# Kernel tuning notes

Hardware: AMD Instinct MI355X
Metric: run time of the kernel (lower is better)

The kernel has to match this reference:

```python
import jax, jax.numpy as jnp
import numpy as np

B = 8192
D_LS, D_A, D_LM, D_AT, D_DS, D_DM = 1024, 512, 512, 512, 1024, 512
LENGTH = D_LS + D_A + D_LM  # 2048
OUT = 512


def setup_inputs() -> dict:
    key = jax.random.key(0)
    ks = jax.random.split(key, 9)
    return {
        "result_ls": jax.random.normal(ks[0], (B, 1, D_LS), jnp.float32),
        "result_A": jax.random.normal(ks[1], (B, 1, D_A), jnp.float32),
        "result_lm": jax.random.normal(ks[2], (B, 1, D_LM), jnp.float32),
        "result_AT": jax.random.normal(ks[3], (B, 1, D_AT), jnp.float32),
        "result_ds": jax.random.normal(ks[4], (B, 1, D_DS), jnp.float32),
        "result_dm": jax.random.normal(ks[5], (B, 1, D_DM), jnp.float32),
        "W": jax.random.normal(ks[6], (OUT, LENGTH), jnp.float32) * (1.0 / np.sqrt(LENGTH)),
        "b": jax.random.normal(ks[7], (OUT,), jnp.float32) * 0.01,
        "h_n": jax.random.normal(ks[8], (OUT, 1), jnp.float32) * (1.0 / np.sqrt(OUT)),
    }


def _pad_to(x, length):
    # zero-pad last dim of [B,1,d] to [B,1,length]
    return jnp.pad(x, ((0, 0), (0, 0), (0, length - x.shape[2])))


def reference(result_ls, result_A, result_lm, result_AT, result_ds, result_dm, W, b, h_n):
    # pad each node-type feature to common length and stack along node axis -> [B,6,L]
    nodes = jnp.concatenate(
        [_pad_to(t, LENGTH) for t in (result_ls, result_A, result_lm, result_AT, result_ds, result_dm)],
        axis=1,
    )
    temp = jnp.tanh(jnp.einsum("bnl,ol->bno", nodes, W) + b)  # [B,6,OUT]
    score = jnp.einsum("bno,oi->bni", temp, h_n)               # [B,6,1]
    score = score.reshape(-1, 1, 6)
    beta = jax.nn.softmax(score, axis=2)                        # [B,1,6]
    z_i = jnp.matmul(beta, nodes)                               # [B,1,L]
    return z_i
```

## Files before the change

### kernel.cpp

```cpp
#include <hip/hip_runtime.h>
#include <hip/hip_bf16.h>
#include <stdint.h>

typedef __attribute__((ext_vector_type(8))) short bf16x8;
typedef __attribute__((ext_vector_type(4))) float f32x4;

#define NB 8192

__device__ __forceinline__ unsigned pkbf(float x, float y) {
    __hip_bfloat162 h = __float22bfloat162_rn(make_float2(x, y));
    unsigned r;
    __builtin_memcpy(&r, &h, 4);
    return r;
}

__device__ __forceinline__ uint4 pack8(float4 a, float4 b) {
    uint4 r;
    r.x = pkbf(a.x, a.y);
    r.y = pkbf(a.z, a.w);
    r.z = pkbf(b.x, b.y);
    r.w = pkbf(b.z, b.w);
    return r;
}

__global__ __launch_bounds__(256)
void prep_w_kernel(const float* __restrict__ W, uint4* __restrict__ Wt) {
    int t = blockIdx.x * 256 + threadIdx.x;
    int lane = t & 63;
    int frag = t >> 6;
    int kb = frag >> 5, cb = frag & 31;
    int o = cb * 16 + (lane & 15);
    int k = kb * 32 + ((lane >> 4) << 3);
    const float* src = W + (size_t)o * 2048 + k;
    Wt[t] = pack8(*(const float4*)src, *(const float4*)(src + 4));
}

template<int DN>
__device__ __forceinline__ void score_body(
        const float* __restrict__ xp, int node, int tile,
        const float* __restrict__ bias, const float* __restrict__ hvec,
        const uint4* __restrict__ Wt, float* __restrict__ scores,
        uint4* lA, float* red) {
    constexpr int NKH = DN / 512;
    int t = threadIdx.x;
    int l = t & 63;
    int w = t >> 6;
    int m0 = tile << 6;

    f32x4 acc[4][4];
#pragma unroll
    for (int mf = 0; mf < 4; ++mf)
#pragma unroll
        for (int nf = 0; nf < 4; ++nf)
            acc[mf][nf] = (f32x4){0.f, 0.f, 0.f, 0.f};

    for (int kh = 0; kh < NKH; ++kh) {
        if (kh > 0) __syncthreads();
#pragma unroll
        for (int j = 0; j < 8; ++j) {
            int f = (t >> 6) + (j << 3);
            int row = (f & 3) * 16 + (l & 15);
            int k = (kh << 9) + ((f >> 2) << 5) + ((l >> 4) << 3);
            const float* g = xp + (size_t)(m0 + row) * DN + k;
            lA[(f << 6) + l] = pack8(*(const float4*)g, *(const float4*)(g + 4));
        }
        __syncthreads();

        int kbh0 = w << 1;
        uint4 bB[2][4], aA[2][4];
        {
            int kbh = kbh0 & 15;
            const uint4* wp = Wt + ((((kh << 4) + kbh) * 32 + (w << 2)) << 6) + l;
#pragma unroll
            for (int nf = 0; nf < 4; ++nf) bB[0][nf] = wp[nf << 6];
#pragma unroll
            for (int mf = 0; mf < 4; ++mf) aA[0][mf] = lA[(((kbh << 2) + mf) << 6) + l];
        }
#pragma unroll
        for (int i = 0; i < 16; ++i) {
            int cur = i & 1, nxt = cur ^ 1;
            if (i < 15) {
                int kbh = (kbh0 + i + 1) & 15;
                const uint4* wp = Wt + ((((kh << 4) + kbh) * 32 + (w << 2)) << 6) + l;
#pragma unroll
                for (int nf = 0; nf < 4; ++nf) bB[nxt][nf] = wp[nf << 6];
#pragma unroll
                for (int mf = 0; mf < 4; ++mf) aA[nxt][mf] = lA[(((kbh << 2) + mf) << 6) + l];
            }
#pragma unroll
            for (int mf = 0; mf < 4; ++mf) {
                bf16x8 afr;
                __builtin_memcpy(&afr, &aA[cur][mf], 16);
#pragma unroll
                for (int nf = 0; nf < 4; ++nf) {
                    bf16x8 bfr;
                    __builtin_memcpy(&bfr, &bB[cur][nf], 16);
                    acc[mf][nf] = __builtin_amdgcn_mfma_f32_16x16x32_bf16(
                        afr, bfr, acc[mf][nf], 0, 0, 0);
                }
            }
        }
    }

    float bv[4], hv[4];
#pragma unroll
    for (int nf = 0; nf < 4; ++nf) {
        int o = (w << 6) + (nf << 4) + (l & 15);
        bv[nf] = bias[o];
        hv[nf] = hvec[o];
    }
#pragma unroll
    for (int mf = 0; mf < 4; ++mf) {
        float sc[4] = {0.f, 0.f, 0.f, 0.f};
#pragma unroll
        for (int nf = 0; nf < 4; ++nf) {
#pragma unroll
            for (int r = 0; r < 4; ++r) {
                float xv = acc[mf][nf][r] + bv[nf];
                float th = 1.f - 2.f * __builtin_amdgcn_rcpf(1.f + __expf(2.f * xv));
                sc[r] = fmaf(hv[nf], th, sc[r]);
            }
        }
#pragma unroll
        for (int r = 0; r < 4; ++r) {
            float v = sc[r];
            v += __shfl_xor(v, 1);
            v += __shfl_xor(v, 2);
            v += __shfl_xor(v, 4);
            v += __shfl_xor(v, 8);
            if ((l & 15) == 0)
                red[(w << 6) + (mf << 4) + ((l >> 4) << 2) + r] = v;
        }
    }
    __syncthreads();
    if (t < 64) {
        float ssum = 0.f;
#pragma unroll
        for (int w2 = 0; w2 < 8; ++w2) ssum += red[(w2 << 6) + t];
        scores[node * NB + m0 + t] = ssum;
    }
}

__global__ __launch_bounds__(512)
void score_kernel(const float* __restrict__ x0, const float* __restrict__ x1,
                  const float* __restrict__ x2, const float* __restrict__ x3,
                  const float* __restrict__ x4, const float* __restrict__ x5,
                  const float* __restrict__ bias, const float* __restrict__ hvec,
                  const uint4* __restrict__ Wt, float* __restrict__ scores) {
    __shared__ uint4 lA[4096];
    __shared__ float red[8 * 64];
    int bid = blockIdx.x;
    int node = bid % 6;
    int tile = bid / 6;
    switch (node) {
        case 0: score_body<1024>(x0, 0, tile, bias, hvec, Wt, scores, lA, red); break;
        case 1: score_body<512>(x1, 1, tile, bias, hvec, Wt, scores, lA, red); break;
        case 2: score_body<512>(x2, 2, tile, bias, hvec, Wt, scores, lA, red); break;
        case 3: score_body<512>(x3, 3, tile, bias, hvec, Wt, scores, lA, red); break;
        case 4: score_body<1024>(x4, 4, tile, bias, hvec, Wt, scores, lA, red); break;
        default: score_body<512>(x5, 5, tile, bias, hvec, Wt, scores, lA, red); break;
    }
}

__global__ __launch_bounds__(256)
void z_kernel(const float* __restrict__ x0, const float* __restrict__ x1,
              const float* __restrict__ x2, const float* __restrict__ x3,
              const float* __restrict__ x4, const float* __restrict__ x5,
              const float* __restrict__ scores, float* __restrict__ out) {
    int wv = threadIdx.x >> 6;
    int lane = threadIdx.x & 63;
    int b = (blockIdx.x << 2) + wv;

    float s0 = scores[b];
    float s1 = scores[NB + b];
    float s2 = scores[2 * NB + b];
    float s3 = scores[3 * NB + b];
    float s4 = scores[4 * NB + b];
    float s5 = scores[5 * NB + b];
    float m = fmaxf(fmaxf(fmaxf(s0, s1), fmaxf(s2, s3)), fmaxf(s4, s5));
    float e0 = __expf(s0 - m), e1 = __expf(s1 - m), e2 = __expf(s2 - m);
    float e3 = __expf(s3 - m), e4 = __expf(s4 - m), e5 = __expf(s5 - m);
    float inv = __builtin_amdgcn_rcpf(e0 + e1 + e2 + e3 + e4 + e5);
    float b0 = e0 * inv, b1 = e1 * inv, b2 = e2 * inv;
    float b3 = e3 * inv, b4 = e4 * inv, b5 = e5 * inv;

    const float* pls = x0 + (size_t)b * 1024;
    const float* pA  = x1 + (size_t)b * 512;
    const float* plm = x2 + (size_t)b * 512;
    const float* pAT = x3 + (size_t)b * 512;
    const float* pds = x4 + (size_t)b * 1024;
    const float* pdm = x5 + (size_t)b * 512;
    float* po = out + (size_t)b * 2048;

#pragma unroll
    for (int j = 0; j < 2; ++j) {
        int c = (j << 8) + (lane << 2);
        float4 vls = *(const float4*)(pls + c);
        float4 vA  = *(const float4*)(pA + c);
        float4 vlm = *(const float4*)(plm + c);
        float4 vAT = *(const float4*)(pAT + c);
        float4 vds = *(const float4*)(pds + c);
        float4 vdm = *(const float4*)(pdm + c);
        float4 r;
        r.x = b0*vls.x + b1*vA.x + b2*vlm.x + b3*vAT.x + b4*vds.x + b5*vdm.x;
        r.y = b0*vls.y + b1*vA.y + b2*vlm.y + b3*vAT.y + b4*vds.y + b5*vdm.y;
        r.z = b0*vls.z + b1*vA.z + b2*vlm.z + b3*vAT.z + b4*vds.z + b5*vdm.z;
        r.w = b0*vls.w + b1*vA.w + b2*vlm.w + b3*vAT.w + b4*vds.w + b5*vdm.w;
        *(float4*)(po + c) = r;
    }
#pragma unroll
    for (int j = 0; j < 2; ++j) {
        int c = 512 + (j << 8) + (lane << 2);
        float4 vls = *(const float4*)(pls + c);
        float4 vds = *(const float4*)(pds + c);
        float4 r;
        r.x = b0*vls.x + b4*vds.x;
        r.y = b0*vls.y + b4*vds.y;
        r.z = b0*vls.z + b4*vds.z;
        r.w = b0*vls.w + b4*vds.w;
        *(float4*)(po + c) = r;
    }
    float4 zz = make_float4(0.f, 0.f, 0.f, 0.f);
#pragma unroll
    for (int j = 0; j < 4; ++j) {
        int c = 1024 + (j << 8) + (lane << 2);
        *(float4*)(po + c) = zz;
    }
}

extern "C" void kernel_launch(void* const* d_in, const int* in_sizes, int n_in,
                              void* d_out, int out_size, void* d_ws, size_t ws_size,
                              hipStream_t stream) {
    const float* x0   = (const float*)d_in[0];
    const float* x1   = (const float*)d_in[1];
    const float* x2   = (const float*)d_in[2];
    const float* x3   = (const float*)d_in[3];
    const float* x4   = (const float*)d_in[4];
    const float* x5   = (const float*)d_in[5];
    const float* W    = (const float*)d_in[6];
    const float* bias = (const float*)d_in[7];
    const float* hvec = (const float*)d_in[8];

    uint4* Wt = (uint4*)d_ws;
    float* scores = (float*)((char*)d_ws + (1u << 20));

    prep_w_kernel<<<256, 256, 0, stream>>>(W, Wt);
    score_kernel<<<768, 512, 0, stream>>>(x0, x1, x2, x3, x4, x5, bias, hvec, Wt, scores);
    z_kernel<<<2048, 256, 0, stream>>>(x0, x1, x2, x3, x4, x5, scores, (float*)d_out);
}
```

Before: 114.1 us.

## Double-buffer activation tiles via async global-to-LDS loads with swizzle

The score kernel now streams fp32 activation tiles straight into LDS with global_load_lds, double-buffered in 128-column stages using an XOR swizzle. Each wave converts fp32 to bf16 when it reads from LDS, and W fragments are prefetched two k-blocks ahead in a register ring. The goal is to overlap activation loads with MFMA work and to drop the per-half register staging and full __syncthreads round trips. In exchange, LDS use doubles to 64KB, each wave repeats the fp32-to-bf16 packing, and raw s_barrier calls without an explicit wait on the asynchronous LDS loads could be a hazard.

```diff
diff --git a/kernel.cpp b/kernel.cpp
--- a/kernel.cpp
+++ b/kernel.cpp
@@ -21,6 +21,12 @@
     r.z = pkbf(b.x, b.y);
     r.w = pkbf(b.z, b.w);
     return r;
+}
+
+__device__ __forceinline__ void gload16(const float* g, void* l) {
+    __builtin_amdgcn_global_load_lds(
+        (const __attribute__((address_space(1))) void*)g,
+        (__attribute__((address_space(3))) void*)l, 16, 0, 0);
 }
 
 __global__ __launch_bounds__(256)
@@ -40,13 +46,22 @@
         const float* __restrict__ xp, int node, int tile,
         const float* __restrict__ bias, const float* __restrict__ hvec,
         const uint4* __restrict__ Wt, float* __restrict__ scores,
-        uint4* lA, float* red) {
-    constexpr int NKH = DN / 512;
+        char* lds, float* red) {
+    constexpr int NBUF = DN / 128;
+    constexpr int NKB = DN / 32;
     int t = threadIdx.x;
     int l = t & 63;
     int w = t >> 6;
     int m0 = tile << 6;
 
+    int rA[4], gcol[4];
+#pragma unroll
+    for (int i = 0; i < 4; ++i) {
+        int r = (((w << 2) + i) << 1) + (l >> 5);
+        rA[i] = r;
+        gcol[i] = ((l & 31) ^ (r & 7)) << 2;
+    }
+
     f32x4 acc[4][4];
 #pragma unroll
     for (int mf = 0; mf < 4; ++mf)
@@ -54,52 +69,62 @@
         for (int nf = 0; nf < 4; ++nf)
             acc[mf][nf] = (f32x4){0.f, 0.f, 0.f, 0.f};
 
-    for (int kh = 0; kh < NKH; ++kh) {
-        if (kh > 0) __syncthreads();
-#pragma unroll
-        for (int j = 0; j < 8; ++j) {
-            int f = (t >> 6) + (j << 3);
-            int row = (f & 3) * 16 + (l & 15);
-            int k = (kh << 9) + ((f >> 2) << 5) + ((l >> 4) << 3);
-            const float* g = xp + (size_t)(m0 + row) * DN + k;
-            lA[(f << 6) + l] = pack8(*(const float4*)g, *(const float4*)(g + 4));
-        }
-        __syncthreads();
-
-        int kbh0 = w << 1;
-        uint4 bB[2][4], aA[2][4];
-        {
-            int kbh = kbh0 & 15;
-            const uint4* wp = Wt + ((((kh << 4) + kbh) * 32 + (w << 2)) << 6) + l;
-#pragma unroll
-            for (int nf = 0; nf < 4; ++nf) bB[0][nf] = wp[nf << 6];
-#pragma unroll
-            for (int mf = 0; mf < 4; ++mf) aA[0][mf] = lA[(((kbh << 2) + mf) << 6) + l];
-        }
-#pragma unroll
-        for (int i = 0; i < 16; ++i) {
-            int cur = i & 1, nxt = cur ^ 1;
-            if (i < 15) {
-                int kbh = (kbh0 + i + 1) & 15;
-                const uint4* wp = Wt + ((((kh << 4) + kbh) * 32 + (w << 2)) << 6) + l;
-#pragma unroll
-                for (int nf = 0; nf < 4; ++nf) bB[nxt][nf] = wp[nf << 6];
-#pragma unroll
-                for (int mf = 0; mf < 4; ++mf) aA[nxt][mf] = lA[(((kbh << 2) + mf) << 6) + l];
+    uint4 bR[4][4];
+
+#pragma unroll
+    for (int i = 0; i < 4; ++i)
+        gload16(xp + (size_t)(m0 + rA[i]) * DN + gcol[i],
+                lds + (((w << 2) + i) << 10));
+#pragma unroll
+    for (int pk = 0; pk < 2; ++pk) {
+        const uint4* wp = Wt + (((pk << 5) + (w << 2)) << 6) + l;
+#pragma unroll
+        for (int nf = 0; nf < 4; ++nf) bR[pk][nf] = wp[nf << 6];
+    }
+    __syncthreads();
+
+    for (int s = 0; s < NBUF; ++s) {
+        int cur = s & 1;
+        const char* buf = lds + (cur << 15);
+        if (s + 1 < NBUF) {
+            int koff = (s + 1) << 7;
+#pragma unroll
+            for (int i = 0; i < 4; ++i)
+                gload16(xp + (size_t)(m0 + rA[i]) * DN + koff + gcol[i],
+                        lds + ((cur ^ 1) << 15) + (((w << 2) + i) << 10));
+        }
+        __builtin_amdgcn_sched_barrier(0);
+#pragma unroll
+        for (int kbh = 0; kbh < 4; ++kbh) {
+            int kb = (s << 2) + kbh;
+            if (kb + 2 < NKB) {
+                const uint4* wp = Wt + ((((kb + 2) << 5) + (w << 2)) << 6) + l;
+#pragma unroll
+                for (int nf = 0; nf < 4; ++nf) bR[(kbh + 2) & 3][nf] = wp[nf << 6];
             }
 #pragma unroll
             for (int mf = 0; mf < 4; ++mf) {
+                int r = (mf << 4) + (l & 15);
+                int s0 = (kbh << 3) + ((l >> 4) << 1);
+                int sw = r & 7;
+                const char* p = buf + r * 512;
+                float4 lo = *(const float4*)(p + ((s0 ^ sw) << 4));
+                float4 hi = *(const float4*)(p + (((s0 + 1) ^ sw) << 4));
+                uint4 pkd = pack8(lo, hi);
                 bf16x8 afr;
-                __builtin_memcpy(&afr, &aA[cur][mf], 16);
+                __builtin_memcpy(&afr, &pkd, 16);
 #pragma unroll
                 for (int nf = 0; nf < 4; ++nf) {
                     bf16x8 bfr;
-                    __builtin_memcpy(&bfr, &bB[cur][nf], 16);
+                    __builtin_memcpy(&bfr, &bR[kbh & 3][nf], 16);
                     acc[mf][nf] = __builtin_amdgcn_mfma_f32_16x16x32_bf16(
                         afr, bfr, acc[mf][nf], 0, 0, 0);
                 }
             }
         }
+        __builtin_amdgcn_sched_barrier(0);
+        __builtin_amdgcn_s_barrier();
+        __builtin_amdgcn_sched_barrier(0);
     }
 
     float bv[4], hv[4];
@@ -147,18 +172,18 @@
                   const float* __restrict__ x4, const float* __restrict__ x5,
                   const float* __restrict__ bias, const float* __restrict__ hvec,
                   const uint4* __restrict__ Wt, float* __restrict__ scores) {
-    __shared__ uint4 lA[4096];
+    __shared__ char lds[65536];
     __shared__ float red[8 * 64];
     int bid = blockIdx.x;
     int node = bid % 6;
     int tile = bid / 6;
     switch (node) {
-        case 0: score_body<1024>(x0, 0, tile, bias, hvec, Wt, scores, lA, red); break;
-        case 1: score_body<512>(x1, 1, tile, bias, hvec, Wt, scores, lA, red); break;
-        case 2: score_body<512>(x2, 2, tile, bias, hvec, Wt, scores, lA, red); break;
-        case 3: score_body<512>(x3, 3, tile, bias, hvec, Wt, scores, lA, red); break;
-        case 4: score_body<1024>(x4, 4, tile, bias, hvec, Wt, scores, lA, red); break;
-        default: score_body<512>(x5, 5, tile, bias, hvec, Wt, scores, lA, red); break;
+        case 0: score_body<1024>(x0, 0, tile, bias, hvec, Wt, scores, lds, red); break;
+        case 1: score_body<512>(x1, 1, tile, bias, hvec, Wt, scores, lds, red); break;
+        case 2: score_body<512>(x2, 2, tile, bias, hvec, Wt, scores, lds, red); break;
+        case 3: score_body<512>(x3, 3, tile, bias, hvec, Wt, scores, lds, red); break;
+        case 4: score_body<1024>(x4, 4, tile, bias, hvec, Wt, scores, lds, red); break;
+        default: score_body<512>(x5, 5, tile, bias, hvec, Wt, scores, lds, red); break;
     }
 }
 
```

After: 119.7 us. 1.05x slower.
